# Performance work log

Measured on AMD Instinct MI355X. Metric: run time of the kernel, lower is better.

## Reference

```python
import jax, jax.numpy as jnp
import numpy as np

B, QH, KVH, D, P = 32, 32, 8, 128, 4096
N = QH * D
KN = KVH * D


def setup_inputs() -> dict:
    key = jax.random.key(0)
    ks = jax.random.split(key, 6)
    s = np.float32(1.0 / np.sqrt(N))
    return {
        "X": jax.random.normal(ks[0], (B, N), jnp.float32),
        "Wq": jax.random.normal(ks[1], (N, N), jnp.float32) * s,
        "Wk": jax.random.normal(ks[2], (KN, N), jnp.float32) * s,
        "Wv": jax.random.normal(ks[3], (KN, N), jnp.float32) * s,
        # scale cache so the non-stabilized exp() stays in fp32 range
        "cache_K": jax.random.normal(ks[4], (B, P, KVH, D), jnp.float32) * 0.1,
        "cache_V": jax.random.normal(ks[5], (B, P, KVH, D), jnp.float32),
    }


def reference(X, Wq, Wk, Wv, cache_K, cache_V):
    Bx, Nx = X.shape
    KVHx, Dx = cache_K.shape[2], cache_K.shape[3]
    QHx = Nx // Dx
    G = QHx // KVHx  # GQA group size
    # RMSNorm (no learned scale)
    x2 = jnp.sum(X * X, axis=1, keepdims=True)
    x_norm = X / jnp.sqrt(x2 / Nx)
    q = (x_norm @ Wq.T).reshape(Bx, KVHx, G, Dx)       # [B,KVH,G,D]
    k_new = (x_norm @ Wk.T).reshape(Bx, 1, KVHx, Dx)
    v_new = (x_norm @ Wv.T).reshape(Bx, 1, KVHx, Dx)
    k_cache = jnp.concatenate([cache_K, k_new], axis=1)  # [B,S,KVH,D], S=P+1
    v_cache = jnp.concatenate([cache_V, v_new], axis=1)
    # GQA: q head h = kv*G + g attends kv head kv (== repeat_interleave)
    scores = jnp.einsum("bkgd,bskd->bkgs", q, k_cache)  # [B,KVH,G,S]
    e = jnp.exp(scores)  # faithful non-stabilized softmax
    attn = e / jnp.sum(e, axis=3, keepdims=True)
    o = jnp.einsum("bkgs,bskd->bkgd", attn, v_cache)     # [B,KVH,G,D]
    return o.reshape(Bx, Nx)
```

## Files before the change

### kernel.cpp

```cpp
#include <hip/hip_runtime.h>

constexpr int kB    = 32;
constexpr int kKVH  = 8;
constexpr int kD    = 128;
constexpr int kP    = 4096;
constexpr int kN    = 4096;
constexpr int kKN   = 1024;
constexpr int kG    = 4;
constexpr int kNS   = 2;
constexpr int kSplit = kP / kNS;
constexpr int kChunk = 64;
constexpr int kStride = 130;

__global__ __launch_bounds__(256) void rms_norm_kernel(const float* __restrict__ X,
                                                       float* __restrict__ xn) {
  int b = blockIdx.x;
  const float4* x4 = (const float4*)(X + (size_t)b * kN);
  float4* o4 = (float4*)(xn + (size_t)b * kN);
  float ss = 0.f;
  float4 v[4];
#pragma unroll
  for (int i = 0; i < 4; ++i) {
    v[i] = x4[threadIdx.x + i * 256];
    ss += v[i].x * v[i].x + v[i].y * v[i].y + v[i].z * v[i].z + v[i].w * v[i].w;
  }
#pragma unroll
  for (int m = 32; m; m >>= 1) ss += __shfl_xor(ss, m, 64);
  __shared__ float red[4];
  if ((threadIdx.x & 63) == 0) red[threadIdx.x >> 6] = ss;
  __syncthreads();
  float total = red[0] + red[1] + red[2] + red[3];
  float scale = rsqrtf(total * (1.f / kN));
#pragma unroll
  for (int i = 0; i < 4; ++i) {
    float4 r;
    r.x = v[i].x * scale; r.y = v[i].y * scale;
    r.z = v[i].z * scale; r.w = v[i].w * scale;
    o4[threadIdx.x + i * 256] = r;
  }
}

__global__ __launch_bounds__(256) void qkv_gemm_kernel(
    const float* __restrict__ xn, const float* __restrict__ Wq,
    const float* __restrict__ Wk, const float* __restrict__ Wv,
    float* __restrict__ qb, float* __restrict__ knew, float* __restrict__ vnew) {
  __shared__ float Wt[32 * 68];
  __shared__ float Xt[32 * 68];
  int c0 = blockIdx.x * 32;
  const float* wsel;
  float* outp;
  int ostride;
  if (c0 < kN) {
    wsel = Wq + (size_t)c0 * kN; outp = qb + c0; ostride = kN;
  } else if (c0 < kN + kKN) {
    wsel = Wk + (size_t)(c0 - kN) * kN; outp = knew + (c0 - kN); ostride = kKN;
  } else {
    wsel = Wv + (size_t)(c0 - kN - kKN) * kN; outp = vnew + (c0 - kN - kKN); ostride = kKN;
  }
  int t = threadIdx.x;
  int cl = t & 31;
  int bg = t >> 5;
  int sr = t >> 3;
  int sp = t & 7;
  float acc0 = 0.f, acc1 = 0.f, acc2 = 0.f, acc3 = 0.f;
  for (int k0 = 0; k0 < kN; k0 += 64) {
    __syncthreads();
    {
      const float4* wsrc = (const float4*)(wsel + (size_t)sr * kN + k0 + sp * 8);
      float4 w0 = wsrc[0], w1 = wsrc[1];
      const float4* xsrc = (const float4*)(xn + (size_t)sr * kN + k0 + sp * 8);
      float4 x0 = xsrc[0], x1 = xsrc[1];
      float4* wdst = (float4*)(Wt + sr * 68 + sp * 8);
      wdst[0] = w0; wdst[1] = w1;
      float4* xdst = (float4*)(Xt + sr * 68 + sp * 8);
      xdst[0] = x0; xdst[1] = x1;
    }
    __syncthreads();
    const float* wrow = Wt + cl * 68;
    const float* xr0 = Xt + (bg * 4 + 0) * 68;
    const float* xr1 = Xt + (bg * 4 + 1) * 68;
    const float* xr2 = Xt + (bg * 4 + 2) * 68;
    const float* xr3 = Xt + (bg * 4 + 3) * 68;
#pragma unroll
    for (int kk = 0; kk < 64; kk += 4) {
      float4 w4 = *(const float4*)(wrow + kk);
      float4 a0 = *(const float4*)(xr0 + kk);
      float4 a1 = *(const float4*)(xr1 + kk);
      float4 a2 = *(const float4*)(xr2 + kk);
      float4 a3 = *(const float4*)(xr3 + kk);
      acc0 += w4.x * a0.x + w4.y * a0.y + w4.z * a0.z + w4.w * a0.w;
      acc1 += w4.x * a1.x + w4.y * a1.y + w4.z * a1.z + w4.w * a1.w;
      acc2 += w4.x * a2.x + w4.y * a2.y + w4.z * a2.z + w4.w * a2.w;
      acc3 += w4.x * a3.x + w4.y * a3.y + w4.z * a3.z + w4.w * a3.w;
    }
  }
  outp[(size_t)(bg * 4 + 0) * ostride + cl] = acc0;
  outp[(size_t)(bg * 4 + 1) * ostride + cl] = acc1;
  outp[(size_t)(bg * 4 + 2) * ostride + cl] = acc2;
  outp[(size_t)(bg * 4 + 3) * ostride + cl] = acc3;
}

__global__ __launch_bounds__(256) void attn_partial_kernel(
    const float* __restrict__ cK, const float* __restrict__ cV,
    const float* __restrict__ qb, float* __restrict__ num, float* __restrict__ den) {
  __shared__ float Kt[kChunk * kStride];
  __shared__ float Vt[kChunk * kStride];
  __shared__ float qs[kG * kD];
  int blk = blockIdx.x;
  int ss = blk & (kNS - 1);
  int kv = (blk >> 1) & (kKVH - 1);
  int b  = blk >> 4;
  int t = threadIdx.x;
  int w = t >> 6;
  int l = t & 63;
  for (int i = t; i < kG * kD; i += 256) {
    int g = i >> 7, d = i & 127;
    qs[i] = qb[(size_t)b * kN + (kv * kG + g) * kD + d];
  }
  const float* Kbase = cK + ((size_t)b * kP + (size_t)ss * kSplit) * kKN + kv * kD;
  const float* Vbase = cV + ((size_t)b * kP + (size_t)ss * kSplit) * kKN + kv * kD;
  float o0 = 0.f, o1 = 0.f, denp = 0.f;
  for (int c0 = 0; c0 < kSplit; c0 += kChunk) {
    __syncthreads();
    for (int i = t; i < kChunk * 32; i += 256) {
      int s = i >> 5, dq = (i & 31) * 4;
      float4 k4 = *(const float4*)(Kbase + (size_t)(c0 + s) * kKN + dq);
      float4 v4 = *(const float4*)(Vbase + (size_t)(c0 + s) * kKN + dq);
      float* kd = Kt + s * kStride + dq;
      *(float2*)(kd)     = make_float2(k4.x, k4.y);
      *(float2*)(kd + 2) = make_float2(k4.z, k4.w);
      float* vd = Vt + s * kStride + dq;
      *(float2*)(vd)     = make_float2(v4.x, v4.y);
      *(float2*)(vd + 2) = make_float2(v4.z, v4.w);
    }
    __syncthreads();
    const float* krow = Kt + l * kStride;
    const float* qrow = qs + w * kD;
    float sc = 0.f;
#pragma unroll
    for (int d = 0; d < kD; d += 4) {
      float4 q4 = *(const float4*)(qrow + d);
      sc += q4.x * krow[d] + q4.y * krow[d + 1] + q4.z * krow[d + 2] + q4.w * krow[d + 3];
    }
    float e = __expf(sc);
    denp += e;
#pragma unroll 16
    for (int s = 0; s < kChunk; ++s) {
      float es = __shfl(e, s, 64);
      float2 v2 = *(const float2*)(Vt + s * kStride + l * 2);
      o0 += es * v2.x;
      o1 += es * v2.y;
    }
  }
  size_t base = ((((size_t)ss * kB + b) * kKVH + kv) * kG + w) * kD;
  num[base + l * 2]     = o0;
  num[base + l * 2 + 1] = o1;
#pragma unroll
  for (int m = 32; m; m >>= 1) denp += __shfl_xor(denp, m, 64);
  if (l == 0) den[(((size_t)ss * kB + b) * kKVH + kv) * kG + w] = denp;
}

__global__ __launch_bounds__(256) void attn_final_kernel(
    const float* __restrict__ qb, const float* __restrict__ knew,
    const float* __restrict__ vnew, const float* __restrict__ num,
    const float* __restrict__ den, float* __restrict__ out) {
  int blk = blockIdx.x;
  int kv = blk & (kKVH - 1);
  int b  = blk >> 3;
  int t = threadIdx.x;
  int g = t >> 6, l = t & 63;
  const float* qrow = qb + (size_t)b * kN + (kv * kG + g) * kD;
  const float* krow = knew + (size_t)b * kKN + kv * kD;
  const float* vrow = vnew + (size_t)b * kKN + kv * kD;
  float2 q2 = *(const float2*)(qrow + l * 2);
  float2 k2 = *(const float2*)(krow + l * 2);
  float dot = q2.x * k2.x + q2.y * k2.y;
#pragma unroll
  for (int m = 32; m; m >>= 1) dot += __shfl_xor(dot, m, 64);
  float e = __expf(dot);
  size_t p0 = (((size_t)0 * kB + b) * kKVH + kv) * kG + g;
  size_t p1 = (((size_t)1 * kB + b) * kKVH + kv) * kG + g;
  float dtot = den[p0] + den[p1] + e;
  float2 v2 = *(const float2*)(vrow + l * 2);
  float n0 = num[p0 * kD + l * 2]     + num[p1 * kD + l * 2]     + e * v2.x;
  float n1 = num[p0 * kD + l * 2 + 1] + num[p1 * kD + l * 2 + 1] + e * v2.y;
  float inv = 1.f / dtot;
  float* orow = out + (size_t)b * kN + (kv * kG + g) * kD;
  orow[l * 2]     = n0 * inv;
  orow[l * 2 + 1] = n1 * inv;
}

extern "C" void kernel_launch(void* const* d_in, const int* in_sizes, int n_in,
                              void* d_out, int out_size, void* d_ws, size_t ws_size,
                              hipStream_t stream) {
  const float* X  = (const float*)d_in[0];
  const float* Wq = (const float*)d_in[1];
  const float* Wk = (const float*)d_in[2];
  const float* Wv = (const float*)d_in[3];
  const float* cK = (const float*)d_in[4];
  const float* cV = (const float*)d_in[5];
  float* out = (float*)d_out;

  float* ws   = (float*)d_ws;
  float* xn   = ws;
  float* qb   = xn + (size_t)kB * kN;
  float* knew = qb + (size_t)kB * kN;
  float* vnew = knew + (size_t)kB * kKN;
  float* num  = vnew + (size_t)kB * kKN;
  float* den  = num + (size_t)kNS * kB * kKVH * kG * kD;

  hipLaunchKernelGGL(rms_norm_kernel, dim3(kB), dim3(256), 0, stream, X, xn);
  hipLaunchKernelGGL(qkv_gemm_kernel, dim3((kN + 2 * kKN) / 32), dim3(256), 0, stream,
                     xn, Wq, Wk, Wv, qb, knew, vnew);
  hipLaunchKernelGGL(attn_partial_kernel, dim3(kB * kKVH * kNS), dim3(256), 0, stream,
                     cK, cV, qb, num, den);
  hipLaunchKernelGGL(attn_final_kernel, dim3(kB * kKVH), dim3(256), 0, stream,
                     qb, knew, vnew, num, den, out);
}
```

Measured before the change: 1.206 ms.

## Register-prefetch next tiles in QKV GEMM and attention, widen V accumulation to float4

Both the QKV projection and the attention-partial kernel now load the next global tile into registers while computing on the current shared-memory tile, so global latency overlaps with compute. The attention kernel also pads K/V rows to a 16-byte-aligned stride for float4 shared stores and reads. Its PV loop has each half-wave take alternate rows with float4 accumulators, combined by a final cross-half shuffle. This adds register pressure (16 float4 prefetch registers), which the launch-bounds hint of 2 blocks per SM is meant to keep in check.

```diff
diff --git a/kernel.cpp b/kernel.cpp
--- a/kernel.cpp
+++ b/kernel.cpp
@@ -10,7 +10,7 @@
 constexpr int kNS   = 2;
 constexpr int kSplit = kP / kNS;
 constexpr int kChunk = 64;
-constexpr int kStride = 130;
+constexpr int kStride = 132;
 
 __global__ __launch_bounds__(256) void rms_norm_kernel(const float* __restrict__ X,
                                                        float* __restrict__ xn) {
@@ -62,20 +62,26 @@
   int bg = t >> 5;
   int sr = t >> 3;
   int sp = t & 7;
+  const float* wsrc = wsel + (size_t)sr * kN + sp * 8;
+  const float* xsrc = xn + (size_t)sr * kN + sp * 8;
+  float4 w0 = *(const float4*)(wsrc);
+  float4 w1 = *(const float4*)(wsrc + 4);
+  float4 x0 = *(const float4*)(xsrc);
+  float4 x1 = *(const float4*)(xsrc + 4);
   float acc0 = 0.f, acc1 = 0.f, acc2 = 0.f, acc3 = 0.f;
   for (int k0 = 0; k0 < kN; k0 += 64) {
     __syncthreads();
-    {
-      const float4* wsrc = (const float4*)(wsel + (size_t)sr * kN + k0 + sp * 8);
-      float4 w0 = wsrc[0], w1 = wsrc[1];
-      const float4* xsrc = (const float4*)(xn + (size_t)sr * kN + k0 + sp * 8);
-      float4 x0 = xsrc[0], x1 = xsrc[1];
-      float4* wdst = (float4*)(Wt + sr * 68 + sp * 8);
-      wdst[0] = w0; wdst[1] = w1;
-      float4* xdst = (float4*)(Xt + sr * 68 + sp * 8);
-      xdst[0] = x0; xdst[1] = x1;
-    }
-    __syncthreads();
+    *(float4*)(Wt + sr * 68 + sp * 8)     = w0;
+    *(float4*)(Wt + sr * 68 + sp * 8 + 4) = w1;
+    *(float4*)(Xt + sr * 68 + sp * 8)     = x0;
+    *(float4*)(Xt + sr * 68 + sp * 8 + 4) = x1;
+    __syncthreads();
+    if (k0 + 64 < kN) {
+      w0 = *(const float4*)(wsrc + k0 + 64);
+      w1 = *(const float4*)(wsrc + k0 + 68);
+      x0 = *(const float4*)(xsrc + k0 + 64);
+      x1 = *(const float4*)(xsrc + k0 + 68);
+    }
     const float* wrow = Wt + cl * 68;
     const float* xr0 = Xt + (bg * 4 + 0) * 68;
     const float* xr1 = Xt + (bg * 4 + 1) * 68;
@@ -100,7 +106,7 @@
   outp[(size_t)(bg * 4 + 3) * ostride + cl] = acc3;
 }
 
-__global__ __launch_bounds__(256) void attn_partial_kernel(
+__global__ __launch_bounds__(256, 2) void attn_partial_kernel(
     const float* __restrict__ cK, const float* __restrict__ cV,
     const float* __restrict__ qb, float* __restrict__ num, float* __restrict__ den) {
   __shared__ float Kt[kChunk * kStride];
@@ -114,47 +120,64 @@
   int w = t >> 6;
   int l = t & 63;
   for (int i = t; i < kG * kD; i += 256) {
-    int g = i >> 7, d = i & 127;
-    qs[i] = qb[(size_t)b * kN + (kv * kG + g) * kD + d];
-  }
-  const float* Kbase = cK + ((size_t)b * kP + (size_t)ss * kSplit) * kKN + kv * kD;
-  const float* Vbase = cV + ((size_t)b * kP + (size_t)ss * kSplit) * kKN + kv * kD;
-  float o0 = 0.f, o1 = 0.f, denp = 0.f;
+    qs[i] = qb[(size_t)b * kN + kv * kG * kD + i];
+  }
+  int srow = t >> 5;
+  int qd   = (t & 31) * 4;
+  const float* Kb = cK + ((size_t)b * kP + (size_t)ss * kSplit) * kKN + kv * kD + qd;
+  const float* Vb = cV + ((size_t)b * kP + (size_t)ss * kSplit) * kKN + kv * kD + qd;
+  float4 kreg[8], vreg[8];
+#pragma unroll
+  for (int j = 0; j < 8; ++j) {
+    kreg[j] = *(const float4*)(Kb + (size_t)(srow + 8 * j) * kKN);
+    vreg[j] = *(const float4*)(Vb + (size_t)(srow + 8 * j) * kKN);
+  }
+  float4 acc = make_float4(0.f, 0.f, 0.f, 0.f);
+  float denp = 0.f;
+  int half = l >> 5;
   for (int c0 = 0; c0 < kSplit; c0 += kChunk) {
     __syncthreads();
-    for (int i = t; i < kChunk * 32; i += 256) {
-      int s = i >> 5, dq = (i & 31) * 4;
-      float4 k4 = *(const float4*)(Kbase + (size_t)(c0 + s) * kKN + dq);
-      float4 v4 = *(const float4*)(Vbase + (size_t)(c0 + s) * kKN + dq);
-      float* kd = Kt + s * kStride + dq;
-      *(float2*)(kd)     = make_float2(k4.x, k4.y);
-      *(float2*)(kd + 2) = make_float2(k4.z, k4.w);
-      float* vd = Vt + s * kStride + dq;
-      *(float2*)(vd)     = make_float2(v4.x, v4.y);
-      *(float2*)(vd + 2) = make_float2(v4.z, v4.w);
-    }
-    __syncthreads();
+#pragma unroll
+    for (int j = 0; j < 8; ++j) {
+      *(float4*)(Kt + (srow + 8 * j) * kStride + qd) = kreg[j];
+      *(float4*)(Vt + (srow + 8 * j) * kStride + qd) = vreg[j];
+    }
+    __syncthreads();
+    if (c0 + kChunk < kSplit) {
+      const float* Kn = Kb + (size_t)(c0 + kChunk) * kKN;
+      const float* Vn = Vb + (size_t)(c0 + kChunk) * kKN;
+#pragma unroll
+      for (int j = 0; j < 8; ++j) {
+        kreg[j] = *(const float4*)(Kn + (size_t)(srow + 8 * j) * kKN);
+        vreg[j] = *(const float4*)(Vn + (size_t)(srow + 8 * j) * kKN);
+      }
+    }
     const float* krow = Kt + l * kStride;
     const float* qrow = qs + w * kD;
     float sc = 0.f;
 #pragma unroll
-    for (int d = 0; d < kD; d += 4) {
-      float4 q4 = *(const float4*)(qrow + d);
-      sc += q4.x * krow[d] + q4.y * krow[d + 1] + q4.z * krow[d + 2] + q4.w * krow[d + 3];
+    for (int q = 0; q < 32; ++q) {
+      float4 k4 = *(const float4*)(krow + q * 4);
+      float4 q4 = *(const float4*)(qrow + q * 4);
+      sc += k4.x * q4.x + k4.y * q4.y + k4.z * q4.z + k4.w * q4.w;
     }
     float e = __expf(sc);
     denp += e;
-#pragma unroll 16
-    for (int s = 0; s < kChunk; ++s) {
-      float es = __shfl(e, s, 64);
-      float2 v2 = *(const float2*)(Vt + s * kStride + l * 2);
-      o0 += es * v2.x;
-      o1 += es * v2.y;
-    }
-  }
+    const float* vq = Vt + half * kStride + qd;
+#pragma unroll
+    for (int i = 0; i < 32; ++i) {
+      float es = __shfl(e, 2 * i + half, 64);
+      float4 v4 = *(const float4*)(vq + i * (2 * kStride));
+      acc.x += es * v4.x; acc.y += es * v4.y;
+      acc.z += es * v4.z; acc.w += es * v4.w;
+    }
+  }
+  acc.x += __shfl_xor(acc.x, 32, 64);
+  acc.y += __shfl_xor(acc.y, 32, 64);
+  acc.z += __shfl_xor(acc.z, 32, 64);
+  acc.w += __shfl_xor(acc.w, 32, 64);
   size_t base = ((((size_t)ss * kB + b) * kKVH + kv) * kG + w) * kD;
-  num[base + l * 2]     = o0;
-  num[base + l * 2 + 1] = o1;
+  if (l < 32) *(float4*)(num + base + qd) = acc;
 #pragma unroll
   for (int m = 32; m; m >>= 1) denp += __shfl_xor(denp, m, 64);
   if (l == 0) den[(((size_t)ss * kB + b) * kKVH + kv) * kG + w] = denp;
```

Measured after the change: 1.340 ms. 1.11x slower.
